# Performance work log

Measured on AMD Instinct MI355X. Metric: run time of the kernel, lower is better.

The kernel has to match this reference:

```python
import jax, jax.numpy as jnp
import numpy as np

K_NN = 5
COS_EPS = 1e-8  # torch cosine_similarity eps


def setup_inputs() -> dict:
    key = jax.random.key(0)
    ks = jax.random.split(key, 10)
    N1, N2, D, E, H = 2000, 2000, 63, 64, 8
    return {
        "lm_X": jax.random.normal(ks[0], (N1, D), jnp.float32),
        "lm_Y": jax.random.normal(ks[1], (N1, 2), jnp.float32),
        "tg_X": jax.random.normal(ks[2], (N2, D), jnp.float32),
        "tg_Y": jax.random.normal(ks[3], (N2, 2), jnp.float32),
        "lm_delay": jax.random.uniform(ks[4], (N1,), jnp.float32),
        "tg_delay": jax.random.uniform(ks[5], (N2,), jnp.float32),
        # learned params: embedding Linear(input_dim=D+1 -> E) and per-head score weights
        "W_emb": jax.random.normal(ks[6], (E, D + 1), jnp.float32) / np.sqrt(D + 1),
        "b_emb": jnp.zeros((E,), jnp.float32),
        "w1": jax.random.normal(ks[7], (E, H), jnp.float32),
        "w2": jax.random.normal(ks[8], (E, H), jnp.float32),
    }


def _knn_adj(X, k):
    # binary row-wise k-nearest-neighbour adjacency, self excluded
    n = X.shape[0]
    sq = jnp.sum(X * X, axis=1)
    d2 = sq[:, None] + sq[None, :] - 2.0 * (X @ X.T)  # [n, n] squared distances
    d2 = jnp.where(jnp.eye(n, dtype=bool), jnp.inf, d2)  # exclude self
    _, idx = jax.lax.top_k(-d2, k)  # k smallest distances -> [n, k]
    rows = jnp.arange(n)[:, None]
    return jnp.zeros((n, n), X.dtype).at[rows, idx].set(1.0)


def reference(lm_X, lm_Y, tg_X, tg_Y, lm_delay, tg_delay, W_emb, b_emb, w1, w2):
    N1 = lm_X.shape[0]
    N2 = tg_X.shape[0]
    N = N1 + N2
    k = K_NN

    # ---- community-KNN adjacency over landmarks, label aggregation ----
    adj_lm = _knn_adj(lm_X, k)                      # [N1, N1] binary, k ones per row
    y_pred = (adj_lm @ lm_Y) * (1.0 / k)            # [N1, 2]

    # ---- teacher adjacency: (1 - I) with lm block = adj_lm, tg block = 0 ----
    adj_teacher = 1.0 - jnp.eye(N, dtype=lm_X.dtype)
    adj_teacher = adj_teacher.at[:N1, :N1].set(adj_lm)
    adj_teacher = adj_teacher.at[N1:, N1:].set(0.0)

    # ---- node features + embedding ----
    lm_feat = jnp.concatenate([lm_X, lm_delay[:, None]], axis=1)  # [N1, D+1]
    tg_feat = jnp.concatenate([tg_X, tg_delay[:, None]], axis=1)  # [N2, D+1]
    feats = jnp.concatenate([lm_feat, tg_feat], axis=0)           # [N, D+1]
    e = feats @ W_emb.T + b_emb                                    # [N, E]

    # ---- multi-head cosine-similarity edge probabilities (all heads at once) ----
    a = e[:, None, :] * w1.T[None, :, :]            # [N, H, E] : e * w1[:, h]
    b = e[:, None, :] * w2.T[None, :, :]            # [N, H, E] : e * w2[:, h]
    na = jnp.linalg.norm(a, axis=-1)                # [N, H]
    nb = jnp.linalg.norm(b, axis=-1)                # [N, H]
    dot = jnp.einsum("nhe,mhe->nmh", a, b)          # [N, N, H]
    sim = dot / jnp.maximum(na[:, None, :] * nb[None, :, :], COS_EPS)
    alpha = jax.nn.sigmoid(sim)                      # [N, N, H]
    adj = jnp.mean(alpha, axis=-1)                   # [N, N]

    return (y_pred, adj, adj_teacher)
```

## Files before the change

### kernel.cpp

```cpp
#include <hip/hip_runtime.h>
#include <math.h>

#define N1 2000
#define N2 2000
#define NT 4000
#define D  63
#define E  64
#define H  8
#define KNN 5
#define NPAD 4032
#define MPAD 4096
#define NWIN 32

typedef short bf16x8 __attribute__((ext_vector_type(8)));
typedef float f32x4  __attribute__((ext_vector_type(4)));

__device__ __forceinline__ unsigned short f2bf(float x) {
    unsigned u = __float_as_uint(x);
    u = (u + 0x7fffu + ((u >> 16) & 1u)) >> 16;
    return (unsigned short)u;
}

__device__ __forceinline__ bool dless(float d1, int i1, float d2v, int i2) {
    return d1 < d2v || (d1 == d2v && i1 < i2);
}

__device__ __forceinline__ void ins5(float bd[KNN], int bi[KNN], float d, int j) {
    if (dless(d, j, bd[KNN - 1], bi[KNN - 1])) {
        bd[KNN - 1] = d; bi[KNN - 1] = j;
        #pragma unroll
        for (int s = KNN - 1; s > 0; --s) {
            if (dless(bd[s], bi[s], bd[s - 1], bi[s - 1])) {
                float td = bd[s]; bd[s] = bd[s - 1]; bd[s - 1] = td;
                int ti = bi[s]; bi[s] = bi[s - 1]; bi[s - 1] = ti;
            }
        }
    }
}

__global__ __launch_bounds__(256) void k_knn(const float* __restrict__ X,
                                             float* __restrict__ part_d,
                                             int* __restrict__ part_i) {
    __shared__ float Xi[64][68];
    __shared__ float Xj[64][68];
    __shared__ float sqi[64];
    __shared__ float sqj[64];
    int cb = blockIdx.x, rb = blockIdx.y;
    int i0 = rb * 64, j0 = cb * 64;
    int tid = threadIdx.x;

    for (int t = tid; t < 64 * 64; t += 256) {
        int r = t >> 6, c = t & 63;
        int gi = min(i0 + r, N1 - 1);
        int gj = min(j0 + r, N1 - 1);
        Xi[r][c] = (c < D) ? X[gi * D + c] : 0.f;
        Xj[r][c] = (c < D) ? X[gj * D + c] : 0.f;
    }
    __syncthreads();
    if (tid < 128) {
        int r = tid & 63;
        const float* src = (tid < 64) ? &Xi[r][0] : &Xj[r][0];
        float s = 0.f;
        #pragma unroll
        for (int q = 0; q < 16; ++q) {
            float4 v = *(const float4*)&src[4 * q];
            s += v.x * v.x + v.y * v.y + v.z * v.z + v.w * v.w;
        }
        if (tid < 64) sqi[r] = s; else sqj[r] = s;
    }
    __syncthreads();

    int tx = tid & 15, ty = tid >> 4;
    float acc[4][4];
    #pragma unroll
    for (int a = 0; a < 4; ++a)
        #pragma unroll
        for (int b = 0; b < 4; ++b) acc[a][b] = 0.f;

    #pragma unroll 4
    for (int kk = 0; kk < 16; ++kk) {
        float4 av[4], bv[4];
        #pragma unroll
        for (int ii = 0; ii < 4; ++ii) av[ii] = *(const float4*)&Xi[ty + 16 * ii][4 * kk];
        #pragma unroll
        for (int jj = 0; jj < 4; ++jj) bv[jj] = *(const float4*)&Xj[tx + 16 * jj][4 * kk];
        #pragma unroll
        for (int ii = 0; ii < 4; ++ii)
            #pragma unroll
            for (int jj = 0; jj < 4; ++jj)
                acc[ii][jj] += av[ii].x * bv[jj].x + av[ii].y * bv[jj].y +
                               av[ii].z * bv[jj].z + av[ii].w * bv[jj].w;
    }

    float bd[4][KNN]; int bi[4][KNN];
    #pragma unroll
    for (int ii = 0; ii < 4; ++ii) {
        #pragma unroll
        for (int s = 0; s < KNN; ++s) { bd[ii][s] = __builtin_inff(); bi[ii][s] = 0x7fffffff; }
        int gi = i0 + ty + 16 * ii;
        float si = sqi[ty + 16 * ii];
        #pragma unroll
        for (int jj = 0; jj < 4; ++jj) {
            int gj = j0 + tx + 16 * jj;
            if (gj < N1 && gj != gi) {
                float dv = si + sqj[tx + 16 * jj] - 2.f * acc[ii][jj];
                ins5(bd[ii], bi[ii], dv, gj);
            }
        }
    }

    #pragma unroll
    for (int ii = 0; ii < 4; ++ii) {
        float wd[KNN]; int wi[KNN];
        #pragma unroll
        for (int s = 0; s < KNN; ++s) {
            float d = bd[ii][0]; int ix = bi[ii][0];
            #pragma unroll
            for (int m = 1; m < 16; m <<= 1) {
                float od = __shfl_xor(d, m, 64);
                int   oi = __shfl_xor(ix, m, 64);
                if (dless(od, oi, d, ix)) { d = od; ix = oi; }
            }
            wd[s] = d; wi[s] = ix;
            if (d == bd[ii][0] && ix == bi[ii][0]) {
                #pragma unroll
                for (int q = 0; q < KNN - 1; ++q) { bd[ii][q] = bd[ii][q + 1]; bi[ii][q] = bi[ii][q + 1]; }
                bd[ii][KNN - 1] = __builtin_inff(); bi[ii][KNN - 1] = 0x7fffffff;
            }
        }
        if (tx == 0) {
            int row = i0 + ty + 16 * ii;
            if (row < N1) {
                #pragma unroll
                for (int s = 0; s < KNN; ++s) {
                    part_d[row * (NWIN * KNN) + cb * KNN + s] = wd[s];
                    part_i[row * (NWIN * KNN) + cb * KNN + s] = wi[s];
                }
            }
        }
    }
}

__global__ __launch_bounds__(256) void k_mgprep(const float* __restrict__ part_d,
                                                const int* __restrict__ part_i,
                                                const float* __restrict__ lmY,
                                                float* __restrict__ ypred,
                                                int* __restrict__ idx,
                                                const float* __restrict__ lmX,
                                                const float* __restrict__ tgX,
                                                const float* __restrict__ lmD,
                                                const float* __restrict__ tgD,
                                                const float* __restrict__ W,
                                                const float* __restrict__ bias,
                                                const float* __restrict__ w1,
                                                const float* __restrict__ w2,
                                                unsigned short* __restrict__ AL,
                                                unsigned short* __restrict__ Bbuf,
                                                float* __restrict__ sB) {
    int tid = threadIdx.x, lane = tid & 63, wave = tid >> 6;

    if (blockIdx.x < 500) {
        int row = blockIdx.x * 4 + wave;
        float ld[3]; int li[3];
        #pragma unroll
        for (int q = 0; q < 3; ++q) {
            int c = lane + 64 * q;
            if (c < NWIN * KNN) {
                ld[q] = part_d[row * (NWIN * KNN) + c];
                li[q] = part_i[row * (NWIN * KNN) + c];
            } else { ld[q] = __builtin_inff(); li[q] = 0x7fffffff; }
        }
        #pragma unroll
        for (int a = 0; a < 2; ++a)
            #pragma unroll
            for (int q = 0; q < 2; ++q)
                if (dless(ld[q + 1], li[q + 1], ld[q], li[q])) {
                    float td = ld[q]; ld[q] = ld[q + 1]; ld[q + 1] = td;
                    int ti = li[q]; li[q] = li[q + 1]; li[q + 1] = ti;
                }
        float d = ld[0]; int ix = li[0]; int p = 0;
        float rd[KNN]; int ri[KNN];
        #pragma unroll
        for (int s = 0; s < KNN; ++s) {
            float md = d; int mi = ix;
            #pragma unroll
            for (int m = 1; m < 64; m <<= 1) {
                float od = __shfl_xor(md, m, 64);
                int   oi = __shfl_xor(mi, m, 64);
                if (dless(od, oi, md, mi)) { md = od; mi = oi; }
            }
            rd[s] = md; ri[s] = mi;
            if (md == d && mi == ix) {
                ++p;
                d  = (p < 3) ? ld[p] : __builtin_inff();
                ix = (p < 3) ? li[p] : 0x7fffffff;
            }
        }
        if (lane == 0) {
            float y0 = 0.f, y1 = 0.f;
            #pragma unroll
            for (int s = 0; s < KNN; ++s) {
                int j = ri[s];
                y0 += lmY[j * 2];
                y1 += lmY[j * 2 + 1];
                idx[row * KNN + s] = j;
            }
            ypred[row * 2]     = y0 * 0.2f;
            ypred[row * 2 + 1] = y1 * 0.2f;
        }
    }

    __shared__ float f[4][E];
    __shared__ float Wl[E][68];
    int n = blockIdx.x * 4 + wave;
    #pragma unroll
    for (int k = 0; k < 4; ++k) {
        int g = k * 256 + tid;
        float4 v = ((const float4*)W)[g];
        int r = g >> 4, c = (g & 15) * 4;
        *(float4*)&Wl[r][c] = v;
    }
    int t = lane;
    if (t < D)  f[wave][t] = (n < N1) ? lmX[n * D + t] : tgX[(n - N1) * D + t];
    if (t == D) f[wave][t] = (n < N1) ? lmD[n] : tgD[n - N1];
    __syncthreads();
    float s0 = 0.f, s1 = 0.f, s2 = 0.f, s3 = 0.f;
    #pragma unroll
    for (int k = 0; k < 16; ++k) {
        float4 wv = *(const float4*)&Wl[t][4 * k];
        float4 fv = *(const float4*)&f[wave][4 * k];
        s0 += fv.x * wv.x; s1 += fv.y * wv.y; s2 += fv.z * wv.z; s3 += fv.w * wv.w;
    }
    const float en = bias[t] + (s0 + s1) + (s2 + s3);
    Bbuf[n * E + t] = f2bf(en);

    int kc = t >> 5, kq = (t >> 3) & 3, j = t & 7;
    int alane = kq * 16 + (n & 15);
    int nb = n >> 4;
    #pragma unroll
    for (int h = 0; h < H; ++h) {
        float a = en * w1[t * H + h];
        float b = en * w2[t * H + h];
        float na2 = a * a, nb2 = b * b;
        #pragma unroll
        for (int m = 32; m >= 1; m >>= 1) {
            na2 += __shfl_xor(na2, m, 64);
            nb2 += __shfl_xor(nb2, m, 64);
        }
        float val = a * w2[t * H + h] * rsqrtf(na2);
        AL[(((nb * 8 + h) << 1) + kc) * 512 + alane * 8 + j] = f2bf(val);
        if (t == h) sB[n * H + h] = rsqrtf(nb2);
    }
}

__global__ __launch_bounds__(256, 4) void k_adjm(const unsigned short* __restrict__ AL,
                                                 const unsigned short* __restrict__ Bbuf,
                                                 const float* __restrict__ sB,
                                                 const int* __restrict__ idx,
                                                 float* __restrict__ adj,
                                                 float* __restrict__ adjT) {
    __shared__ unsigned short Bt[256][68];
    int tid = threadIdx.x;
    int m0 = blockIdx.x * 256, n0 = blockIdx.y * 64;

    #pragma unroll
    for (int it = 0; it < 8; ++it) {
        int g = it * 256 + tid;
        int row = g >> 3, c = g & 7;
        *(bf16x8*)&Bt[row][c * 8] = *(const bf16x8*)&Bbuf[(m0 + row) * E + c * 8];
    }

    int wave = tid >> 6, lane = tid & 63;
    int l15 = lane & 15, kq = lane >> 4;
    int nb = blockIdx.y * 4 + wave;

    bf16x8 afr[H][2];
    #pragma unroll
    for (int h = 0; h < H; ++h)
        #pragma unroll
        for (int kc = 0; kc < 2; ++kc)
            afr[h][kc] = *(const bf16x8*)&AL[(((nb * 8 + h) << 1) + kc) * 512 + lane * 8];

    __syncthreads();

    int nebase = n0 + wave * 16 + kq * 4;

    #pragma unroll 1
    for (int mt = 0; mt < 16; ++mt) {
        int mrow = mt * 16 + l15;
        int mcol = m0 + mrow;
        bf16x8 b0 = *(const bf16x8*)&Bt[mrow][kq * 8];
        bf16x8 b1 = *(const bf16x8*)&Bt[mrow][32 + kq * 8];

        float sum[4] = {0.f, 0.f, 0.f, 0.f};
        #pragma unroll
        for (int hh = 0; hh < 2; ++hh) {
            float sbv[4];
            *(f32x4*)&sbv[0] = *(const f32x4*)&sB[mcol * H + hh * 4];
            f32x4 acc[4];
            #pragma unroll
            for (int h4 = 0; h4 < 4; ++h4) {
                int h = hh * 4 + h4;
                acc[h4] = (f32x4){0.f, 0.f, 0.f, 0.f};
                acc[h4] = __builtin_amdgcn_mfma_f32_16x16x32_bf16(afr[h][0], b0, acc[h4], 0, 0, 0);
                acc[h4] = __builtin_amdgcn_mfma_f32_16x16x32_bf16(afr[h][1], b1, acc[h4], 0, 0, 0);
            }
            #pragma unroll
            for (int reg = 0; reg < 4; ++reg) {
                #pragma unroll
                for (int h4 = 0; h4 < 4; ++h4) {
                    float x = acc[h4][reg] * sbv[h4];
                    float u = x * x;
                    float p = fmaf(u, 1.8919e-3f, -2.0833333e-2f);
                    p = fmaf(u, p, 0.25f);
                    sum[reg] = fmaf(x, p, sum[reg]);
                }
            }
        }

        bool mok = (mcol < NT);
        #pragma unroll
        for (int reg = 0; reg < 4; ++reg) {
            int ne = nebase + reg;
            if (mok && ne < NT) adj[ne * NT + mcol] = fmaf(sum[reg], 0.125f, 0.5f);
        }
    }

    #pragma unroll
    for (int it = 0; it < 16; ++it) {
        int g = it * 256 + tid;
        int r = g >> 6;
        int col = m0 + (g & 63) * 4;
        int row = n0 + r;
        if (row < NT && col < NT) {
            float v = ((row < N1) != (col < N1)) ? 1.f : 0.f;
            float4 o = {v, v, v, v};
            *(float4*)&adjT[row * NT + col] = o;
        }
    }
    __syncthreads();
    for (int p = tid; p < 64 * KNN; p += 256) {
        int r = p / KNN, s = p - r * KNN;
        int row = n0 + r;
        if (row < N1) {
            int jx = idx[row * KNN + s];
            if (jx >= m0 && jx < m0 + 256) adjT[row * NT + jx] = 1.f;
        }
    }
}

extern "C" void kernel_launch(void* const* d_in, const int* in_sizes, int n_in,
                              void* d_out, int out_size, void* d_ws, size_t ws_size,
                              hipStream_t stream) {
    const float* lmX  = (const float*)d_in[0];
    const float* lmY  = (const float*)d_in[1];
    const float* tgX  = (const float*)d_in[2];
    const float* lmD  = (const float*)d_in[4];
    const float* tgD  = (const float*)d_in[5];
    const float* Wemb = (const float*)d_in[6];
    const float* bemb = (const float*)d_in[7];
    const float* w1   = (const float*)d_in[8];
    const float* w2   = (const float*)d_in[9];

    float* out   = (float*)d_out;
    float* ypred = out;
    float* adj   = out + 4000;
    float* adjT  = out + 4000 + 16000000;

    char* ws = (char*)d_ws;
    unsigned short* AL    = (unsigned short*)ws;
    unsigned short* Bbuf  = (unsigned short*)(ws + 4128768);
    float*          sB    = (float*)(ws + 4128768 + 524288);
    float*          partd = (float*)(ws + 4784128);
    int*            parti = (int*)  (ws + 6064128);
    int*            idx   = (int*)  (ws + 7344128);

    dim3 gk(NWIN, 32);
    k_knn<<<gk, 256, 0, stream>>>(lmX, partd, parti);
    k_mgprep<<<NT / 4, 256, 0, stream>>>(partd, parti, lmY, ypred, idx,
                                         lmX, tgX, lmD, tgD, Wemb, bemb, w1, w2,
                                         AL, Bbuf, sB);
    dim3 ga(MPAD / 256, NPAD / 64);
    k_adjm<<<ga, 256, 0, stream>>>(AL, Bbuf, sB, idx, adj, adjT);
}
```

Baseline: 211.0 us.

## Fuse KNN partial search with embedding prep; move KNN merge into adjacency kernel

```diff
diff --git a/kernel.cpp b/kernel.cpp
--- a/kernel.cpp
+++ b/kernel.cpp
@@ -38,228 +38,179 @@
     }
 }
 
-__global__ __launch_bounds__(256) void k_knn(const float* __restrict__ X,
-                                             float* __restrict__ part_d,
-                                             int* __restrict__ part_i) {
-    __shared__ float Xi[64][68];
-    __shared__ float Xj[64][68];
-    __shared__ float sqi[64];
-    __shared__ float sqj[64];
-    int cb = blockIdx.x, rb = blockIdx.y;
-    int i0 = rb * 64, j0 = cb * 64;
-    int tid = threadIdx.x;
-
-    for (int t = tid; t < 64 * 64; t += 256) {
-        int r = t >> 6, c = t & 63;
-        int gi = min(i0 + r, N1 - 1);
-        int gj = min(j0 + r, N1 - 1);
-        Xi[r][c] = (c < D) ? X[gi * D + c] : 0.f;
-        Xj[r][c] = (c < D) ? X[gj * D + c] : 0.f;
-    }
-    __syncthreads();
-    if (tid < 128) {
-        int r = tid & 63;
-        const float* src = (tid < 64) ? &Xi[r][0] : &Xj[r][0];
-        float s = 0.f;
-        #pragma unroll
-        for (int q = 0; q < 16; ++q) {
-            float4 v = *(const float4*)&src[4 * q];
-            s += v.x * v.x + v.y * v.y + v.z * v.z + v.w * v.w;
-        }
-        if (tid < 64) sqi[r] = s; else sqj[r] = s;
-    }
-    __syncthreads();
-
-    int tx = tid & 15, ty = tid >> 4;
-    float acc[4][4];
-    #pragma unroll
-    for (int a = 0; a < 4; ++a)
-        #pragma unroll
-        for (int b = 0; b < 4; ++b) acc[a][b] = 0.f;
-
-    #pragma unroll 4
-    for (int kk = 0; kk < 16; ++kk) {
-        float4 av[4], bv[4];
-        #pragma unroll
-        for (int ii = 0; ii < 4; ++ii) av[ii] = *(const float4*)&Xi[ty + 16 * ii][4 * kk];
-        #pragma unroll
-        for (int jj = 0; jj < 4; ++jj) bv[jj] = *(const float4*)&Xj[tx + 16 * jj][4 * kk];
-        #pragma unroll
-        for (int ii = 0; ii < 4; ++ii)
-            #pragma unroll
-            for (int jj = 0; jj < 4; ++jj)
-                acc[ii][jj] += av[ii].x * bv[jj].x + av[ii].y * bv[jj].y +
-                               av[ii].z * bv[jj].z + av[ii].w * bv[jj].w;
-    }
-
-    float bd[4][KNN]; int bi[4][KNN];
-    #pragma unroll
-    for (int ii = 0; ii < 4; ++ii) {
-        #pragma unroll
-        for (int s = 0; s < KNN; ++s) { bd[ii][s] = __builtin_inff(); bi[ii][s] = 0x7fffffff; }
-        int gi = i0 + ty + 16 * ii;
-        float si = sqi[ty + 16 * ii];
-        #pragma unroll
-        for (int jj = 0; jj < 4; ++jj) {
-            int gj = j0 + tx + 16 * jj;
-            if (gj < N1 && gj != gi) {
-                float dv = si + sqj[tx + 16 * jj] - 2.f * acc[ii][jj];
-                ins5(bd[ii], bi[ii], dv, gj);
-            }
-        }
-    }
-
-    #pragma unroll
-    for (int ii = 0; ii < 4; ++ii) {
-        float wd[KNN]; int wi[KNN];
-        #pragma unroll
-        for (int s = 0; s < KNN; ++s) {
-            float d = bd[ii][0]; int ix = bi[ii][0];
-            #pragma unroll
-            for (int m = 1; m < 16; m <<= 1) {
-                float od = __shfl_xor(d, m, 64);
-                int   oi = __shfl_xor(ix, m, 64);
-                if (dless(od, oi, d, ix)) { d = od; ix = oi; }
-            }
-            wd[s] = d; wi[s] = ix;
-            if (d == bd[ii][0] && ix == bi[ii][0]) {
-                #pragma unroll
-                for (int q = 0; q < KNN - 1; ++q) { bd[ii][q] = bd[ii][q + 1]; bi[ii][q] = bi[ii][q + 1]; }
-                bd[ii][KNN - 1] = __builtin_inff(); bi[ii][KNN - 1] = 0x7fffffff;
-            }
-        }
-        if (tx == 0) {
-            int row = i0 + ty + 16 * ii;
-            if (row < N1) {
-                #pragma unroll
-                for (int s = 0; s < KNN; ++s) {
-                    part_d[row * (NWIN * KNN) + cb * KNN + s] = wd[s];
-                    part_i[row * (NWIN * KNN) + cb * KNN + s] = wi[s];
-                }
-            }
-        }
-    }
-}
-
-__global__ __launch_bounds__(256) void k_mgprep(const float* __restrict__ part_d,
-                                                const int* __restrict__ part_i,
-                                                const float* __restrict__ lmY,
-                                                float* __restrict__ ypred,
-                                                int* __restrict__ idx,
-                                                const float* __restrict__ lmX,
-                                                const float* __restrict__ tgX,
-                                                const float* __restrict__ lmD,
-                                                const float* __restrict__ tgD,
-                                                const float* __restrict__ W,
-                                                const float* __restrict__ bias,
-                                                const float* __restrict__ w1,
-                                                const float* __restrict__ w2,
-                                                unsigned short* __restrict__ AL,
-                                                unsigned short* __restrict__ Bbuf,
-                                                float* __restrict__ sB) {
+__global__ __launch_bounds__(256) void k_knn_prep(
+        const float* __restrict__ X,
+        float* __restrict__ part_d,
+        int* __restrict__ part_i,
+        const float* __restrict__ lmX,
+        const float* __restrict__ tgX,
+        const float* __restrict__ lmD,
+        const float* __restrict__ tgD,
+        const float* __restrict__ W,
+        const float* __restrict__ bias,
+        const float* __restrict__ w1,
+        const float* __restrict__ w2,
+        unsigned short* __restrict__ AL,
+        unsigned short* __restrict__ Bbuf,
+        float* __restrict__ sB) {
+    __shared__ __attribute__((aligned(16))) char smem[35328];
     int tid = threadIdx.x, lane = tid & 63, wave = tid >> 6;
-
-    if (blockIdx.x < 500) {
-        int row = blockIdx.x * 4 + wave;
-        float ld[3]; int li[3];
-        #pragma unroll
-        for (int q = 0; q < 3; ++q) {
-            int c = lane + 64 * q;
-            if (c < NWIN * KNN) {
-                ld[q] = part_d[row * (NWIN * KNN) + c];
-                li[q] = part_i[row * (NWIN * KNN) + c];
-            } else { ld[q] = __builtin_inff(); li[q] = 0x7fffffff; }
-        }
-        #pragma unroll
-        for (int a = 0; a < 2; ++a)
-            #pragma unroll
-            for (int q = 0; q < 2; ++q)
-                if (dless(ld[q + 1], li[q + 1], ld[q], li[q])) {
-                    float td = ld[q]; ld[q] = ld[q + 1]; ld[q + 1] = td;
-                    int ti = li[q]; li[q] = li[q + 1]; li[q + 1] = ti;
-                }
-        float d = ld[0]; int ix = li[0]; int p = 0;
-        float rd[KNN]; int ri[KNN];
-        #pragma unroll
-        for (int s = 0; s < KNN; ++s) {
-            float md = d; int mi = ix;
-            #pragma unroll
-            for (int m = 1; m < 64; m <<= 1) {
-                float od = __shfl_xor(md, m, 64);
-                int   oi = __shfl_xor(mi, m, 64);
-                if (dless(od, oi, md, mi)) { md = od; mi = oi; }
-            }
-            rd[s] = md; ri[s] = mi;
-            if (md == d && mi == ix) {
-                ++p;
-                d  = (p < 3) ? ld[p] : __builtin_inff();
-                ix = (p < 3) ? li[p] : 0x7fffffff;
-            }
-        }
-        if (lane == 0) {
-            float y0 = 0.f, y1 = 0.f;
+    int b = blockIdx.x;
+
+    if (b < 1024) {
+        float (*Xi)[68] = (float (*)[68])smem;
+        float (*Xj)[68] = (float (*)[68])(smem + 17408);
+        float* sqi = (float*)(smem + 34816);
+        float* sqj = (float*)(smem + 35072);
+        int cb = b & 31, rb = b >> 5;
+        int i0 = rb * 64, j0 = cb * 64;
+
+        for (int t = tid; t < 64 * 64; t += 256) {
+            int r = t >> 6, c = t & 63;
+            int gi = min(i0 + r, N1 - 1);
+            int gj = min(j0 + r, N1 - 1);
+            Xi[r][c] = (c < D) ? X[gi * D + c] : 0.f;
+            Xj[r][c] = (c < D) ? X[gj * D + c] : 0.f;
+        }
+        __syncthreads();
+        if (tid < 128) {
+            int r = tid & 63;
+            const float* src = (tid < 64) ? &Xi[r][0] : &Xj[r][0];
+            float s = 0.f;
+            #pragma unroll
+            for (int q = 0; q < 16; ++q) {
+                float4 v = *(const float4*)&src[4 * q];
+                s += v.x * v.x + v.y * v.y + v.z * v.z + v.w * v.w;
+            }
+            if (tid < 64) sqi[r] = s; else sqj[r] = s;
+        }
+        __syncthreads();
+
+        int tx = tid & 15, ty = tid >> 4;
+        float acc[4][4];
+        #pragma unroll
+        for (int a = 0; a < 4; ++a)
+            #pragma unroll
+            for (int c = 0; c < 4; ++c) acc[a][c] = 0.f;
+
+        #pragma unroll 4
+        for (int kk = 0; kk < 16; ++kk) {
+            float4 av[4], bv[4];
+            #pragma unroll
+            for (int ii = 0; ii < 4; ++ii) av[ii] = *(const float4*)&Xi[ty + 16 * ii][4 * kk];
+            #pragma unroll
+            for (int jj = 0; jj < 4; ++jj) bv[jj] = *(const float4*)&Xj[tx + 16 * jj][4 * kk];
+            #pragma unroll
+            for (int ii = 0; ii < 4; ++ii)
+                #pragma unroll
+                for (int jj = 0; jj < 4; ++jj)
+                    acc[ii][jj] += av[ii].x * bv[jj].x + av[ii].y * bv[jj].y +
+                                   av[ii].z * bv[jj].z + av[ii].w * bv[jj].w;
+        }
+
+        float bd[4][KNN]; int bi[4][KNN];
+        #pragma unroll
+        for (int ii = 0; ii < 4; ++ii) {
+            #pragma unroll
+            for (int s = 0; s < KNN; ++s) { bd[ii][s] = __builtin_inff(); bi[ii][s] = 0x7fffffff; }
+            int gi = i0 + ty + 16 * ii;
+            float si = sqi[ty + 16 * ii];
+            #pragma unroll
+            for (int jj = 0; jj < 4; ++jj) {
+                int gj = j0 + tx + 16 * jj;
+                if (gj < N1 && gj != gi) {
+                    float dv = si + sqj[tx + 16 * jj] - 2.f * acc[ii][jj];
+                    ins5(bd[ii], bi[ii], dv, gj);
+                }
+            }
+        }
+
+        #pragma unroll
+        for (int ii = 0; ii < 4; ++ii) {
+            float wd[KNN]; int wi[KNN];
             #pragma unroll
             for (int s = 0; s < KNN; ++s) {
-                int j = ri[s];
-                y0 += lmY[j * 2];
-                y1 += lmY[j * 2 + 1];
-                idx[row * KNN + s] = j;
-            }
-            ypred[row * 2]     = y0 * 0.2f;
-            ypred[row * 2 + 1] = y1 * 0.2f;
-        }
-    }
-
-    __shared__ float f[4][E];
-    __shared__ float Wl[E][68];
-    int n = blockIdx.x * 4 + wave;
-    #pragma unroll
-    for (int k = 0; k < 4; ++k) {
-        int g = k * 256 + tid;
-        float4 v = ((const float4*)W)[g];
-        int r = g >> 4, c = (g & 15) * 4;
-        *(float4*)&Wl[r][c] = v;
-    }
-    int t = lane;
-    if (t < D)  f[wave][t] = (n < N1) ? lmX[n * D + t] : tgX[(n - N1) * D + t];
-    if (t == D) f[wave][t] = (n < N1) ? lmD[n] : tgD[n - N1];
-    __syncthreads();
-    float s0 = 0.f, s1 = 0.f, s2 = 0.f, s3 = 0.f;
-    #pragma unroll
-    for (int k = 0; k < 16; ++k) {
-        float4 wv = *(const float4*)&Wl[t][4 * k];
-        float4 fv = *(const float4*)&f[wave][4 * k];
-        s0 += fv.x * wv.x; s1 += fv.y * wv.y; s2 += fv.z * wv.z; s3 += fv.w * wv.w;
-    }
-    const float en = bias[t] + (s0 + s1) + (s2 + s3);
-    Bbuf[n * E + t] = f2bf(en);
-
-    int kc = t >> 5, kq = (t >> 3) & 3, j = t & 7;
-    int alane = kq * 16 + (n & 15);
-    int nb = n >> 4;
-    #pragma unroll
-    for (int h = 0; h < H; ++h) {
-        float a = en * w1[t * H + h];
-        float b = en * w2[t * H + h];
-        float na2 = a * a, nb2 = b * b;
-        #pragma unroll
-        for (int m = 32; m >= 1; m >>= 1) {
-            na2 += __shfl_xor(na2, m, 64);
-            nb2 += __shfl_xor(nb2, m, 64);
-        }
-        float val = a * w2[t * H + h] * rsqrtf(na2);
-        AL[(((nb * 8 + h) << 1) + kc) * 512 + alane * 8 + j] = f2bf(val);
-        if (t == h) sB[n * H + h] = rsqrtf(nb2);
+                float d = bd[ii][0]; int ix = bi[ii][0];
+                #pragma unroll
+                for (int m = 1; m < 16; m <<= 1) {
+                    float od = __shfl_xor(d, m, 64);
+                    int   oi = __shfl_xor(ix, m, 64);
+                    if (dless(od, oi, d, ix)) { d = od; ix = oi; }
+                }
+                wd[s] = d; wi[s] = ix;
+                if (d == bd[ii][0] && ix == bi[ii][0]) {
+                    #pragma unroll
+                    for (int q = 0; q < KNN - 1; ++q) { bd[ii][q] = bd[ii][q + 1]; bi[ii][q] = bi[ii][q + 1]; }
+                    bd[ii][KNN - 1] = __builtin_inff(); bi[ii][KNN - 1] = 0x7fffffff;
+                }
+            }
+            if (tx == 0) {
+                int row = i0 + ty + 16 * ii;
+                if (row < N1) {
+                    #pragma unroll
+                    for (int s = 0; s < KNN; ++s) {
+                        part_d[row * (NWIN * KNN) + cb * KNN + s] = wd[s];
+                        part_i[row * (NWIN * KNN) + cb * KNN + s] = wi[s];
+                    }
+                }
+            }
+        }
+    } else {
+        float (*f)[E]   = (float (*)[E])smem;
+        float (*Wl)[68] = (float (*)[68])(smem + 1024);
+        int n = (b - 1024) * 4 + wave;
+        #pragma unroll
+        for (int k = 0; k < 4; ++k) {
+            int g = k * 256 + tid;
+            float4 v = ((const float4*)W)[g];
+            int r = g >> 4, c = (g & 15) * 4;
+            *(float4*)&Wl[r][c] = v;
+        }
+        int t = lane;
+        if (t < D)  f[wave][t] = (n < N1) ? lmX[n * D + t] : tgX[(n - N1) * D + t];
+        if (t == D) f[wave][t] = (n < N1) ? lmD[n] : tgD[n - N1];
+        __syncthreads();
+        float s0 = 0.f, s1 = 0.f, s2 = 0.f, s3 = 0.f;
+        #pragma unroll
+        for (int k = 0; k < 16; ++k) {
+            float4 wv = *(const float4*)&Wl[t][4 * k];
+            float4 fv = *(const float4*)&f[wave][4 * k];
+            s0 += fv.x * wv.x; s1 += fv.y * wv.y; s2 += fv.z * wv.z; s3 += fv.w * wv.w;
+        }
+        const float en = bias[t] + (s0 + s1) + (s2 + s3);
+        Bbuf[n * E + t] = f2bf(en);
+
+        int kc = t >> 5, kq = (t >> 3) & 3, j = t & 7;
+        int alane = kq * 16 + (n & 15);
+        int nb = n >> 4;
+        #pragma unroll
+        for (int h = 0; h < H; ++h) {
+            float a = en * w1[t * H + h];
+            float bb = en * w2[t * H + h];
+            float na2 = a * a, nb2 = bb * bb;
+            #pragma unroll
+            for (int m = 32; m >= 1; m >>= 1) {
+                na2 += __shfl_xor(na2, m, 64);
+                nb2 += __shfl_xor(nb2, m, 64);
+            }
+            float val = a * w2[t * H + h] * rsqrtf(na2);
+            AL[(((nb * 8 + h) << 1) + kc) * 512 + alane * 8 + j] = f2bf(val);
+            if (t == h) sB[n * H + h] = rsqrtf(nb2);
+        }
     }
 }
 
 __global__ __launch_bounds__(256, 4) void k_adjm(const unsigned short* __restrict__ AL,
                                                  const unsigned short* __restrict__ Bbuf,
                                                  const float* __restrict__ sB,
-                                                 const int* __restrict__ idx,
+                                                 const float* __restrict__ part_d,
+                                                 const int* __restrict__ part_i,
+                                                 const float* __restrict__ lmY,
+                                                 float* __restrict__ ypred,
                                                  float* __restrict__ adj,
                                                  float* __restrict__ adjT) {
     __shared__ unsigned short Bt[256][68];
+    __shared__ int sidx[64][KNN];
     int tid = threadIdx.x;
     int m0 = blockIdx.x * 256, n0 = blockIdx.y * 64;
 
@@ -338,12 +289,71 @@
             *(float4*)&adjT[row * NT + col] = o;
         }
     }
+
+    if (n0 < N1) {
+        for (int rr = 0; rr < 16; ++rr) {
+            int r = wave * 16 + rr;
+            int row = n0 + r;
+            if (row < N1) {
+                float ld[3]; int li[3];
+                #pragma unroll
+                for (int q = 0; q < 3; ++q) {
+                    int c = lane + 64 * q;
+                    if (c < NWIN * KNN) {
+                        ld[q] = part_d[row * (NWIN * KNN) + c];
+                        li[q] = part_i[row * (NWIN * KNN) + c];
+                    } else { ld[q] = __builtin_inff(); li[q] = 0x7fffffff; }
+                }
+                #pragma unroll
+                for (int a = 0; a < 2; ++a)
+                    #pragma unroll
+                    for (int q = 0; q < 2; ++q)
+                        if (dless(ld[q + 1], li[q + 1], ld[q], li[q])) {
+                            float td = ld[q]; ld[q] = ld[q + 1]; ld[q + 1] = td;
+                            int ti = li[q]; li[q] = li[q + 1]; li[q + 1] = ti;
+                        }
+                float d = ld[0]; int ix = li[0]; int p = 0;
+                float rd[KNN]; int ri[KNN];
+                #pragma unroll
+                for (int s = 0; s < KNN; ++s) {
+                    float md = d; int mi = ix;
+                    #pragma unroll
+                    for (int m = 1; m < 64; m <<= 1) {
+                        float od = __shfl_xor(md, m, 64);
+                        int   oi = __shfl_xor(mi, m, 64);
+                        if (dless(od, oi, md, mi)) { md = od; mi = oi; }
+                    }
+                    rd[s] = md; ri[s] = mi;
+                    if (md == d && mi == ix) {
+                        ++p;
+                        d  = (p < 3) ? ld[p] : __builtin_inff();
+                        ix = (p < 3) ? li[p] : 0x7fffffff;
+                    }
+                }
+                if (lane == 0) {
+                    #pragma unroll
+                    for (int s = 0; s < KNN; ++s) sidx[r][s] = ri[s];
+                    if (blockIdx.x == 0) {
+                        float y0 = 0.f, y1 = 0.f;
+                        #pragma unroll
+                        for (int s = 0; s < KNN; ++s) {
+                            int j = ri[s];
+                            y0 += lmY[j * 2];
+                            y1 += lmY[j * 2 + 1];
+                        }
+                        ypred[row * 2]     = y0 * 0.2f;
+                        ypred[row * 2 + 1] = y1 * 0.2f;
+                    }
+                }
+            }
+        }
+    }
     __syncthreads();
     for (int p = tid; p < 64 * KNN; p += 256) {
         int r = p / KNN, s = p - r * KNN;
         int row = n0 + r;
         if (row < N1) {
-            int jx = idx[row * KNN + s];
+            int jx = sidx[r][s];
             if (jx >= m0 && jx < m0 + 256) adjT[row * NT + jx] = 1.f;
         }
     }
@@ -373,13 +383,11 @@
     float*          sB    = (float*)(ws + 4128768 + 524288);
     float*          partd = (float*)(ws + 4784128);
     int*            parti = (int*)  (ws + 6064128);
-    int*            idx   = (int*)  (ws + 7344128);
-
-    dim3 gk(NWIN, 32);
-    k_knn<<<gk, 256, 0, stream>>>(lmX, partd, parti);
-    k_mgprep<<<NT / 4, 256, 0, stream>>>(partd, parti, lmY, ypred, idx,
+
+    k_knn_prep<<<2024, 256, 0, stream>>>(lmX, partd, parti,
                                          lmX, tgX, lmD, tgD, Wemb, bemb, w1, w2,
                                          AL, Bbuf, sB);
     dim3 ga(MPAD / 256, NPAD / 64);
-    k_adjm<<<ga, 256, 0, stream>>>(AL, Bbuf, sB, idx, adj, adjT);
-}
+    k_adjm<<<ga, 256, 0, stream>>>(AL, Bbuf, sB, partd, parti, lmY, ypred,
+                                   adj, adjT);
+}
```

Result: slower. 237.6 us (+12.6%).
